# Performance work log

Hardware: AMD Instinct MI355X
Metric: run time of the kernel (lower is better)

Reference implementation:

```python
import jax, jax.numpy as jnp
import numpy as np

WS = 7          # window size per spatial dim
NH = 12         # num heads
DIM = 384       # channels
HD = DIM // NH  # head dim = 32
SCALE = HD ** -0.5
N = WS * WS * WS  # 343 tokens per window
B_ = 128        # windows * batch
NW = 64         # mask windows


def _relative_position_index():
    # Faithful replica of the torch __init__ (including indexing='xy' and the
    # 3*Ws[1]-1 / 2*Ws[1]-1 stride multipliers).
    c = np.arange(WS)
    coords = np.stack(np.meshgrid(c, c, c, indexing='xy'))  # (3, WS, WS, WS)
    cf = coords.reshape(3, -1)                               # (3, N)
    rel = (cf[:, :, None] - cf[:, None, :]).transpose(1, 2, 0).astype(np.int64)
    rel = rel + (WS - 1)
    rel[..., 0] *= 3 * WS - 1
    rel[..., 1] *= 2 * WS - 1
    return rel.sum(-1).astype(np.int32)  # (N, N)


def setup_inputs() -> dict:
    key = jax.random.key(0)
    ks = jax.random.split(key, 8)
    return {
        'skip': jax.random.normal(ks[0], (B_, N, DIM), jnp.float32),
        'x_up': jax.random.normal(ks[1], (B_, N, DIM), jnp.float32),
        'pos_embed': jax.random.normal(ks[2], (B_, N, DIM), jnp.float32),
        'mask': jax.random.normal(ks[3], (NW, N, N), jnp.float32),
        'w_kv': jax.random.normal(ks[4], (2 * DIM, DIM), jnp.float32) * 0.02,
        'b_kv': jnp.zeros((2 * DIM,), jnp.float32),
        'w_proj': jax.random.normal(ks[5], (DIM, DIM), jnp.float32) * 0.02,
        'b_proj': jnp.zeros((DIM,), jnp.float32),
        'bias_table': jax.random.normal(ks[6], ((2 * WS - 1) ** 3, NH), jnp.float32) * 0.02,
        'rpi': jnp.asarray(_relative_position_index()),
    }


def reference(skip, x_up, pos_embed, mask, w_kv, b_kv, w_proj, b_proj, bias_table, rpi):
    B, Ntok, C = skip.shape
    # kv projection from skip: (B, N, 2, H, d)
    kv = (skip @ w_kv.T + b_kv).reshape(B, Ntok, 2, NH, HD)
    k = kv[:, :, 0].transpose(0, 2, 1, 3)  # (B, H, N, d)
    v = kv[:, :, 1].transpose(0, 2, 1, 3)  # (B, H, N, d)
    q = x_up.reshape(B, Ntok, NH, HD).transpose(0, 2, 1, 3) * SCALE  # (B, H, N, d)
    attn = jnp.einsum('bhnd,bhmd->bhnm', q, k)  # (B, H, N, N)
    # relative position bias gather: (N, N, H) -> (H, N, N)
    bias = bias_table[rpi.reshape(-1)].reshape(Ntok, Ntok, NH).transpose(2, 0, 1)
    attn = attn + bias[None]
    # shifted-window mask add
    nW = mask.shape[0]
    attn = attn.reshape(B // nW, nW, NH, Ntok, Ntok) + mask[None, :, None]
    attn = jax.nn.softmax(attn.reshape(B, NH, Ntok, Ntok), axis=-1)
    x = jnp.einsum('bhnm,bhmd->bnhd', attn, v).reshape(B, Ntok, C)
    x = x + pos_embed
    return x @ w_proj.T + b_proj
```

## Files before the change

### kernel.cpp

```cpp
#include <hip/hip_runtime.h>

#define NTOK 343
#define NPAD 352
#define DIM 384
#define NHEAD 12
#define HDIM 32
#define NWIN 64
#define BATCH 128
#define SCALE 0.17677669529663687f
#define LOG2E 1.4426950408889634f
#define SCLG2 (0.17677669529663687f * 1.4426950408889634f)
#define NN 117649
#define MG 88
#define GSTRIDE 1372

typedef __attribute__((ext_vector_type(8))) short bf16x8;
typedef __attribute__((ext_vector_type(4))) short bf16x4;
typedef __attribute__((ext_vector_type(4))) float f32x4;
typedef __attribute__((ext_vector_type(4))) int i32x4;

static __device__ inline short f2bf(float f) {
  union { float f; unsigned u; } v; v.f = f;
  unsigned r = v.u + 0x7fffu + ((v.u >> 16) & 1u);
  return (short)(r >> 16);
}
static __device__ inline float bf2f(short s) {
  union { unsigned u; float f; } v; v.u = ((unsigned)(unsigned short)s) << 16;
  return v.f;
}
static __device__ inline int pack2rn(float lo, float hi) {
  union { float f; unsigned u; } a, b;
  a.f = lo; b.f = hi;
  unsigned au = a.u + 0x8000u;
  unsigned bu = b.u + 0x8000u;
  return (int)__builtin_amdgcn_perm(bu, au, 0x07060302u);
}
static __device__ inline short f2bfrn(float f) {
  union { float f; unsigned u; } v; v.f = f;
  return (short)((v.u + 0x8000u) >> 16);
}
static __device__ inline float fexp2(float x) {
  return __builtin_amdgcn_exp2f(x);
}

#define MFMA16(a, b, c) __builtin_amdgcn_mfma_f32_16x16x32_bf16((a), (b), (c), 0, 0, 0)

__global__ __launch_bounds__(256) void bias_pk_kernel(
    const float* __restrict__ table, const int* __restrict__ rpi,
    short* __restrict__ bias_b4) {
  int idx = blockIdx.x * 256 + threadIdx.x;
  const int total = NHEAD * MG * NTOK * 4;
  if (idx >= total) return;
  int r = idx & 3;
  int t = idx >> 2;
  int q = t % NTOK;
  int u = t / NTOK;
  int g = u % MG;
  int h = u / MG;
  int m = g * 4 + r;
  bias_b4[idx] = (m < NTOK) ? f2bf(table[rpi[q * NTOK + m] * NHEAD + h] * LOG2E)
                            : f2bf(-1e30f);
}

__global__ __launch_bounds__(256) void mask_pk_kernel(
    const float* __restrict__ in, short* __restrict__ mask_b4) {
  int idx = blockIdx.x * 256 + threadIdx.x;
  const int total = NWIN * MG * NTOK * 4;
  if (idx >= total) return;
  int r = idx & 3;
  int t = idx >> 2;
  int q = t % NTOK;
  int u = t / NTOK;
  int g = u % MG;
  int w = u / MG;
  int m = g * 4 + r;
  mask_b4[idx] = (m < NTOK) ? f2bf(in[(size_t)w * NN + q * NTOK + m] * LOG2E) : 0;
}

__global__ __launch_bounds__(256) void cvt_skip_kernel(
    const float* __restrict__ in, short* __restrict__ out, int n8) {
  int i = blockIdx.x * 256 + threadIdx.x;
  if (i >= n8) return;
  f32x4 a = *(const f32x4*)(in + (size_t)i * 8);
  f32x4 b = *(const f32x4*)(in + (size_t)i * 8 + 4);
  bf16x8 o;
#pragma unroll
  for (int j = 0; j < 4; ++j) {
    o[j] = f2bf(a[j]);
    o[j + 4] = f2bf(b[j]);
  }
  *(bf16x8*)(out + (size_t)i * 8) = o;
}

__global__ __launch_bounds__(256) void kv_proj_kernel(
    const short* __restrict__ Xbf, const float* __restrict__ W,
    const float* __restrict__ bkv, short* __restrict__ Kws,
    short* __restrict__ Vws) {
  __shared__ short As[128][40];
  __shared__ short Bs[128][40];
  const int L = blockIdx.x;
  const int xcd = L & 7;
  const int j8 = L >> 3;
  const int wg = ((xcd < 2) ? xcd * 258 : 516 + (xcd - 2) * 257) + j8;
  const int n0 = (wg % 6) * 128;
  const int m0 = (wg / 6) * 128;
  const int tid = threadIdx.x;
  const int lane = tid & 63;
  const int wave = tid >> 6;
  const int wm = (wave >> 1) * 64;
  const int wn = (wave & 1) * 64;
  const int lr = lane & 15;
  const int lk = (lane >> 4) * 8;
  const int c4 = (tid & 7) * 4;
  const int rbase = tid >> 3;
  const int arow = tid >> 2;
  const int acol8 = (tid & 3) * 8;
  const f32x4 zero4 = {0.f, 0.f, 0.f, 0.f};

  f32x4 acc[4][4];
#pragma unroll
  for (int m = 0; m < 4; ++m)
#pragma unroll
    for (int n = 0; n < 4; ++n) acc[m][n] = zero4;

  for (int kk = 0; kk < 12; ++kk) {
    __syncthreads();
    *(bf16x8*)(&As[arow][acol8]) =
        *(const bf16x8*)(Xbf + (size_t)(m0 + arow) * DIM + kk * 32 + acol8);
    *(bf16x8*)(&As[arow + 64][acol8]) =
        *(const bf16x8*)(Xbf + (size_t)(m0 + arow + 64) * DIM + kk * 32 + acol8);
#pragma unroll
    for (int i = 0; i < 4; ++i) {
      int row = rbase + i * 32;
      f32x4 v = *(const f32x4*)(W + (size_t)(n0 + row) * DIM + kk * 32 + c4);
      bf16x4 s4;
#pragma unroll
      for (int j = 0; j < 4; ++j) s4[j] = f2bf(v[j]);
      *(bf16x4*)(&Bs[row][c4]) = s4;
    }
    __syncthreads();
    bf16x8 af[4], bf[4];
#pragma unroll
    for (int m = 0; m < 4; ++m) af[m] = *(const bf16x8*)(&As[wm + m * 16 + lr][lk]);
#pragma unroll
    for (int n = 0; n < 4; ++n) bf[n] = *(const bf16x8*)(&Bs[wn + n * 16 + lr][lk]);
#pragma unroll
    for (int m = 0; m < 4; ++m)
#pragma unroll
      for (int n = 0; n < 4; ++n) acc[m][n] = MFMA16(af[m], bf[n], acc[m][n]);
  }

  const int rq = (lane >> 4) * 4;
#pragma unroll
  for (int n = 0; n < 4; ++n) {
    int gcol = n0 + wn + n * 16 + lr;
    float bias = bkv[gcol];
    int c = (gcol >= DIM) ? (gcol - DIM) : gcol;
    int h = c >> 5;
    int hd = c & 31;
    short* dst = (gcol < DIM) ? Kws : Vws;
#pragma unroll
    for (int m = 0; m < 4; ++m) {
#pragma unroll
      for (int r = 0; r < 4; ++r) {
        int grow = m0 + wm + m * 16 + rq + r;
        int bb = grow / NTOK;
        int tok = grow - bb * NTOK;
        dst[(((size_t)bb * NHEAD + h) * NTOK + tok) * HDIM + hd] =
            f2bf(acc[m][n][r] + bias);
      }
    }
  }
}

__global__ __launch_bounds__(256, 3) void attn_kernel(
    const float* __restrict__ x_up, const short* __restrict__ mask_b4,
    const short* __restrict__ bias_b4, const short* __restrict__ Kws,
    const short* __restrict__ Vws, const float* __restrict__ pos,
    short* __restrict__ attn_out) {
  __shared__ short Ksm[NPAD][40];
  __shared__ short Vp[HDIM][NPAD + 8];
  const int bid = blockIdx.x;
  const int xcd = bid & 7;
  const int jj = bid >> 3;
  const int win = xcd * 8 + jj / 24;
  const int rep = jj - (jj / 24) * 24;
  const int h = rep % NHEAD;
  const int b = win + ((rep >= NHEAD) ? 64 : 0);
  const int tid = threadIdx.x;
  const int wave = tid >> 6;
  const int lane = tid & 63;
  const int lr = lane & 15;
  const int lg = lane >> 4;
  const int koff = lg * 8;
  const int koff_s = koff ^ (lane & 8);
  const f32x4 zero4 = {0.f, 0.f, 0.f, 0.f};

  const short* Kb = Kws + ((size_t)b * NHEAD + h) * NTOK * HDIM;
  const short* Vb = Vws + ((size_t)b * NHEAD + h) * NTOK * HDIM;
  {
    const int c8 = (tid & 3) * 8;
    const int rb = tid >> 2;
    const bf16x8 z8 = {0, 0, 0, 0, 0, 0, 0, 0};
#pragma unroll
    for (int r0 = 0; r0 < 384; r0 += 64) {
      int row = r0 + rb;
      if (row < NPAD) {
        bf16x8 kv = z8;
        if (row < NTOK) kv = *(const bf16x8*)(Kb + row * HDIM + c8);
        *(bf16x8*)(&Ksm[row][c8 ^ (row & 8)]) = kv;
      }
    }
#pragma unroll
    for (int r0 = 0; r0 < 384; r0 += 64) {
      int row = r0 + rb;
      if (row < NPAD) {
        bf16x8 vv = z8;
        if (row < NTOK) vv = *(const bf16x8*)(Vb + row * HDIM + c8);
        int p = (row & ~31) | ((row & 12) << 1) | ((row & 16) >> 2) | (row & 3);
#pragma unroll
        for (int i = 0; i < 8; ++i)
          Vp[c8 + i][p ^ ((c8 + i) & 8)] = vv[i];
      }
    }
  }
  __syncthreads();

  for (int qt = 0; qt < 6; ++qt) {
    const int q0 = qt * 64 + wave * 16;
    if (q0 >= NTOK) continue;
    const int qn = q0 + lr;
    const int qidx = (qn < NTOK) ? qn : (NTOK - 1);
    bf16x8 qf;
    {
      const float* qp = x_up + ((size_t)b * NTOK + qidx) * DIM + h * HDIM + koff;
      f32x4 v0 = *(const f32x4*)qp;
      f32x4 v1 = *(const f32x4*)(qp + 4);
#pragma unroll
      for (int i = 0; i < 4; ++i) {
        qf[i] = f2bfrn(v0[i] * SCLG2);
        qf[i + 4] = f2bfrn(v1[i] * SCLG2);
      }
    }
    const short* bq = bias_b4 + (size_t)h * MG * GSTRIDE + (size_t)lg * GSTRIDE +
                      qidx * 4;
    const short* mq = mask_b4 + (size_t)win * MG * GSTRIDE + (size_t)lg * GSTRIDE +
                      qidx * 4;
    f32x4 s[22];
#pragma unroll
    for (int j = 0; j < 22; ++j) {
      bf16x4 bv = *(const bf16x4*)(bq + (size_t)j * 4 * GSTRIDE);
      bf16x4 mv = *(const bf16x4*)(mq + (size_t)j * 4 * GSTRIDE);
#pragma unroll
      for (int r = 0; r < 4; ++r) s[j][r] = bf2f(bv[r]) + bf2f(mv[r]);
    }
    __builtin_amdgcn_s_setprio(1);
#pragma unroll
    for (int j = 0; j < 22; ++j) {
      bf16x8 kf = *(const bf16x8*)(&Ksm[j * 16 + lr][koff_s]);
      s[j] = MFMA16(kf, qf, s[j]);
    }
    __builtin_amdgcn_s_setprio(0);
    f32x4 sum4 = zero4;
    i32x4 up4[11];
#pragma unroll
    for (int j = 0; j < 22; ++j) {
      f32x4 p;
#pragma unroll
      for (int r = 0; r < 4; ++r) p[r] = fexp2(s[j][r]);
      sum4 += p;
      up4[j >> 1][(j & 1) * 2 + 0] = pack2rn(p[0], p[1]);
      up4[j >> 1][(j & 1) * 2 + 1] = pack2rn(p[2], p[3]);
    }
    float sum = (sum4[0] + sum4[1]) + (sum4[2] + sum4[3]);
    sum += __shfl_xor(sum, 16);
    sum += __shfl_xor(sum, 32);
    const float inv = 1.0f / sum;

    f32x4 o0 = zero4;
    f32x4 o1 = zero4;
    __builtin_amdgcn_s_setprio(1);
#pragma unroll
    for (int kt = 0; kt < 11; ++kt) {
      bf16x8 pf = __builtin_bit_cast(bf16x8, up4[kt]);
      bf16x8 a0 = *(const bf16x8*)(&Vp[lr][kt * 32 + koff_s]);
      bf16x8 a1 = *(const bf16x8*)(&Vp[16 + lr][kt * 32 + koff_s]);
      o0 = MFMA16(a0, pf, o0);
      o1 = MFMA16(a1, pf, o1);
    }
    __builtin_amdgcn_s_setprio(0);
    if (qn < NTOK) {
      const float* pp = pos + ((size_t)b * NTOK + qn) * DIM + h * HDIM + 4 * lg;
      f32x4 p0 = *(const f32x4*)pp;
      f32x4 p1 = *(const f32x4*)(pp + 16);
      short* op = attn_out + ((size_t)b * NTOK + qn) * DIM + h * HDIM + 4 * lg;
      *(int*)(op + 0) = pack2rn(o0[0] * inv + p0[0], o0[1] * inv + p0[1]);
      *(int*)(op + 2) = pack2rn(o0[2] * inv + p0[2], o0[3] * inv + p0[3]);
      *(int*)(op + 16) = pack2rn(o1[0] * inv + p1[0], o1[1] * inv + p1[1]);
      *(int*)(op + 18) = pack2rn(o1[2] * inv + p1[2], o1[3] * inv + p1[3]);
    }
  }
}

__global__ __launch_bounds__(256) void out_proj_kernel(
    const short* __restrict__ Xa, const float* __restrict__ W,
    const float* __restrict__ bpr, float* __restrict__ out) {
  __shared__ short As[128][40];
  __shared__ short Bs[128][40];
  const int L = blockIdx.x;
  const int xcd = L & 7;
  const int j8 = L >> 3;
  const int wg = ((xcd < 5) ? xcd * 129 : 645 + (xcd - 5) * 128) + j8;
  const int n0 = (wg % 3) * 128;
  const int m0 = (wg / 3) * 128;
  const int tid = threadIdx.x;
  const int lane = tid & 63;
  const int wave = tid >> 6;
  const int wm = (wave >> 1) * 64;
  const int wn = (wave & 1) * 64;
  const int lr = lane & 15;
  const int lk = (lane >> 4) * 8;
  const int c4 = (tid & 7) * 4;
  const int rbase = tid >> 3;
  const int arow = tid >> 2;
  const int acol8 = (tid & 3) * 8;
  const f32x4 zero4 = {0.f, 0.f, 0.f, 0.f};

  f32x4 acc[4][4];
#pragma unroll
  for (int m = 0; m < 4; ++m)
#pragma unroll
    for (int n = 0; n < 4; ++n) acc[m][n] = zero4;

  for (int kk = 0; kk < 12; ++kk) {
    __syncthreads();
    *(bf16x8*)(&As[arow][acol8]) =
        *(const bf16x8*)(Xa + (size_t)(m0 + arow) * DIM + kk * 32 + acol8);
    *(bf16x8*)(&As[arow + 64][acol8]) =
        *(const bf16x8*)(Xa + (size_t)(m0 + arow + 64) * DIM + kk * 32 + acol8);
#pragma unroll
    for (int i = 0; i < 4; ++i) {
      int row = rbase + i * 32;
      f32x4 v = *(const f32x4*)(W + (size_t)(n0 + row) * DIM + kk * 32 + c4);
      bf16x4 s4;
#pragma unroll
      for (int j = 0; j < 4; ++j) s4[j] = f2bf(v[j]);
      *(bf16x4*)(&Bs[row][c4]) = s4;
    }
    __syncthreads();
    bf16x8 af[4], bf[4];
#pragma unroll
    for (int m = 0; m < 4; ++m) af[m] = *(const bf16x8*)(&As[wm + m * 16 + lr][lk]);
#pragma unroll
    for (int n = 0; n < 4; ++n) bf[n] = *(const bf16x8*)(&Bs[wn + n * 16 + lr][lk]);
#pragma unroll
    for (int m = 0; m < 4; ++m)
#pragma unroll
      for (int n = 0; n < 4; ++n) acc[m][n] = MFMA16(af[m], bf[n], acc[m][n]);
  }

  const int rq = (lane >> 4) * 4;
#pragma unroll
  for (int n = 0; n < 4; ++n) {
    int gcol = n0 + wn + n * 16 + lr;
    float bias = bpr[gcol];
#pragma unroll
    for (int m = 0; m < 4; ++m) {
#pragma unroll
      for (int r = 0; r < 4; ++r) {
        int grow = m0 + wm + m * 16 + rq + r;
        out[(size_t)grow * DIM + gcol] = acc[m][n][r] + bias;
      }
    }
  }
}

extern "C" void kernel_launch(void* const* d_in, const int* in_sizes, int n_in,
                              void* d_out, int out_size, void* d_ws, size_t ws_size,
                              hipStream_t stream) {
  const float* skip = (const float*)d_in[0];
  const float* x_up = (const float*)d_in[1];
  const float* pos = (const float*)d_in[2];
  const float* mask = (const float*)d_in[3];
  const float* w_kv = (const float*)d_in[4];
  const float* b_kv = (const float*)d_in[5];
  const float* w_proj = (const float*)d_in[6];
  const float* b_proj = (const float*)d_in[7];
  const float* bias_table = (const float*)d_in[8];
  const int* rpi = (const int*)d_in[9];
  float* out = (float*)d_out;

  char* ws = (char*)d_ws;
  const size_t kv_bytes = (size_t)BATCH * NHEAD * NTOK * HDIM * 2;
  const size_t bias_bytes = (size_t)NHEAD * MG * NTOK * 4 * 2;
  const size_t mask_bytes = (size_t)NWIN * MG * NTOK * 4 * 2;
  short* Kws = (short*)ws;
  short* Vws = (short*)(ws + kv_bytes);
  short* bias_b4 = (short*)(ws + 2 * kv_bytes);
  short* mask_b4 = (short*)(ws + 2 * kv_bytes + bias_bytes);
  short* skip_bf = (short*)(ws + 2 * kv_bytes + bias_bytes + mask_bytes);
  short* attn_ws = skip_bf;

  const int bias_total = NHEAD * MG * NTOK * 4;
  const int mask_total = NWIN * MG * NTOK * 4;
  const int n8 = BATCH * NTOK * DIM / 8;
  bias_pk_kernel<<<dim3((bias_total + 255) / 256), dim3(256), 0, stream>>>(
      bias_table, rpi, bias_b4);
  mask_pk_kernel<<<dim3((mask_total + 255) / 256), dim3(256), 0, stream>>>(
      mask, mask_b4);
  cvt_skip_kernel<<<dim3((n8 + 255) / 256), dim3(256), 0, stream>>>(
      skip, skip_bf, n8);
  kv_proj_kernel<<<dim3(2058), dim3(256), 0, stream>>>(skip_bf, w_kv, b_kv,
                                                       Kws, Vws);
  attn_kernel<<<dim3(BATCH * NHEAD), dim3(256), 0, stream>>>(
      x_up, mask_b4, bias_b4, Kws, Vws, pos, attn_ws);
  out_proj_kernel<<<dim3(1029), dim3(256), 0, stream>>>(attn_ws, w_proj,
                                                        b_proj, out);
}
```

Measured before the change: 280.3 us.

## Merge prep kernels, pre-convert weights to bf16, prefetch bias/mask tiles in attention

Replaces the three preprocessing launches with one combined prep kernel that also converts w_kv and w_proj to bf16 once. The projection GEMMs then load bf16 weight tiles directly instead of converting fp32 weights on every tile load. In the attention kernel, bias and mask values for the next query tile are loaded into registers while the current tile is still being computed, so global load latency is hidden. The cost is higher register pressure from the 44 prefetch registers, which may reduce occupancy, plus a little extra workspace.

```diff
diff --git a/kernel.cpp b/kernel.cpp
--- a/kernel.cpp
+++ b/kernel.cpp
@@ -14,19 +14,25 @@
 #define MG 88
 #define GSTRIDE 1372
 
+#define GB 5660
+#define GM 30184
+#define GS 8232
+#define GWK 144
+#define GWP 72
+
 typedef __attribute__((ext_vector_type(8))) short bf16x8;
 typedef __attribute__((ext_vector_type(4))) short bf16x4;
 typedef __attribute__((ext_vector_type(4))) float f32x4;
 typedef __attribute__((ext_vector_type(4))) int i32x4;
+typedef __attribute__((ext_vector_type(2))) int i32x2;
 
 static __device__ inline short f2bf(float f) {
   union { float f; unsigned u; } v; v.f = f;
   unsigned r = v.u + 0x7fffu + ((v.u >> 16) & 1u);
   return (short)(r >> 16);
 }
-static __device__ inline float bf2f(short s) {
-  union { unsigned u; float f; } v; v.u = ((unsigned)(unsigned short)s) << 16;
-  return v.f;
+static __device__ inline float asfu(unsigned u) {
+  union { unsigned u; float f; } v; v.u = u; return v.f;
 }
 static __device__ inline int pack2rn(float lo, float hi) {
   union { float f; unsigned u; } a, b;
@@ -45,41 +51,8 @@
 
 #define MFMA16(a, b, c) __builtin_amdgcn_mfma_f32_16x16x32_bf16((a), (b), (c), 0, 0, 0)
 
-__global__ __launch_bounds__(256) void bias_pk_kernel(
-    const float* __restrict__ table, const int* __restrict__ rpi,
-    short* __restrict__ bias_b4) {
-  int idx = blockIdx.x * 256 + threadIdx.x;
-  const int total = NHEAD * MG * NTOK * 4;
-  if (idx >= total) return;
-  int r = idx & 3;
-  int t = idx >> 2;
-  int q = t % NTOK;
-  int u = t / NTOK;
-  int g = u % MG;
-  int h = u / MG;
-  int m = g * 4 + r;
-  bias_b4[idx] = (m < NTOK) ? f2bf(table[rpi[q * NTOK + m] * NHEAD + h] * LOG2E)
-                            : f2bf(-1e30f);
-}
-
-__global__ __launch_bounds__(256) void mask_pk_kernel(
-    const float* __restrict__ in, short* __restrict__ mask_b4) {
-  int idx = blockIdx.x * 256 + threadIdx.x;
-  const int total = NWIN * MG * NTOK * 4;
-  if (idx >= total) return;
-  int r = idx & 3;
-  int t = idx >> 2;
-  int q = t % NTOK;
-  int u = t / NTOK;
-  int g = u % MG;
-  int w = u / MG;
-  int m = g * 4 + r;
-  mask_b4[idx] = (m < NTOK) ? f2bf(in[(size_t)w * NN + q * NTOK + m] * LOG2E) : 0;
-}
-
-__global__ __launch_bounds__(256) void cvt_skip_kernel(
-    const float* __restrict__ in, short* __restrict__ out, int n8) {
-  int i = blockIdx.x * 256 + threadIdx.x;
+static __device__ inline void cvt8(const float* __restrict__ in,
+                                   short* __restrict__ out, int i, int n8) {
   if (i >= n8) return;
   f32x4 a = *(const f32x4*)(in + (size_t)i * 8);
   f32x4 b = *(const f32x4*)(in + (size_t)i * 8 + 4);
@@ -92,8 +65,48 @@
   *(bf16x8*)(out + (size_t)i * 8) = o;
 }
 
+__global__ __launch_bounds__(256) void prep_kernel(
+    const float* __restrict__ table, const int* __restrict__ rpi,
+    short* __restrict__ bias_b4, const float* __restrict__ mask,
+    short* __restrict__ mask_b4, const float* __restrict__ skip,
+    short* __restrict__ skip_bf, const float* __restrict__ wkv,
+    short* __restrict__ wkv_bf, const float* __restrict__ wproj,
+    short* __restrict__ wproj_bf) {
+  const int g = blockIdx.x;
+  const int tid = threadIdx.x;
+  if (g < GB) {
+    int idx = g * 256 + tid;
+    if (idx >= NHEAD * MG * NTOK * 4) return;
+    int r = idx & 3;
+    int t = idx >> 2;
+    int q = t % NTOK;
+    int u = t / NTOK;
+    int gg = u % MG;
+    int h = u / MG;
+    int m = gg * 4 + r;
+    bias_b4[idx] = (m < NTOK) ? f2bf(table[rpi[q * NTOK + m] * NHEAD + h] * LOG2E)
+                              : f2bf(-1e30f);
+  } else if (g < GB + GM) {
+    int idx = (g - GB) * 256 + tid;
+    int r = idx & 3;
+    int t = idx >> 2;
+    int q = t % NTOK;
+    int u = t / NTOK;
+    int gg = u % MG;
+    int w = u / MG;
+    int m = gg * 4 + r;
+    mask_b4[idx] = (m < NTOK) ? f2bf(mask[(size_t)w * NN + q * NTOK + m] * LOG2E) : 0;
+  } else if (g < GB + GM + GS) {
+    cvt8(skip, skip_bf, (g - GB - GM) * 256 + tid, BATCH * NTOK * DIM / 8);
+  } else if (g < GB + GM + GS + GWK) {
+    cvt8(wkv, wkv_bf, (g - GB - GM - GS) * 256 + tid, 2 * DIM * DIM / 8);
+  } else {
+    cvt8(wproj, wproj_bf, (g - GB - GM - GS - GWK) * 256 + tid, DIM * DIM / 8);
+  }
+}
+
 __global__ __launch_bounds__(256) void kv_proj_kernel(
-    const short* __restrict__ Xbf, const float* __restrict__ W,
+    const short* __restrict__ Xbf, const short* __restrict__ Wbf,
     const float* __restrict__ bkv, short* __restrict__ Kws,
     short* __restrict__ Vws) {
   __shared__ short As[128][40];
@@ -111,8 +124,6 @@
   const int wn = (wave & 1) * 64;
   const int lr = lane & 15;
   const int lk = (lane >> 4) * 8;
-  const int c4 = (tid & 7) * 4;
-  const int rbase = tid >> 3;
   const int arow = tid >> 2;
   const int acol8 = (tid & 3) * 8;
   const f32x4 zero4 = {0.f, 0.f, 0.f, 0.f};
@@ -129,15 +140,10 @@
         *(const bf16x8*)(Xbf + (size_t)(m0 + arow) * DIM + kk * 32 + acol8);
     *(bf16x8*)(&As[arow + 64][acol8]) =
         *(const bf16x8*)(Xbf + (size_t)(m0 + arow + 64) * DIM + kk * 32 + acol8);
-#pragma unroll
-    for (int i = 0; i < 4; ++i) {
-      int row = rbase + i * 32;
-      f32x4 v = *(const f32x4*)(W + (size_t)(n0 + row) * DIM + kk * 32 + c4);
-      bf16x4 s4;
-#pragma unroll
-      for (int j = 0; j < 4; ++j) s4[j] = f2bf(v[j]);
-      *(bf16x4*)(&Bs[row][c4]) = s4;
-    }
+    *(bf16x8*)(&Bs[arow][acol8]) =
+        *(const bf16x8*)(Wbf + (size_t)(n0 + arow) * DIM + kk * 32 + acol8);
+    *(bf16x8*)(&Bs[arow + 64][acol8]) =
+        *(const bf16x8*)(Wbf + (size_t)(n0 + arow + 64) * DIM + kk * 32 + acol8);
     __syncthreads();
     bf16x8 af[4], bf[4];
 #pragma unroll
@@ -226,6 +232,20 @@
   }
   __syncthreads();
 
+  const size_t bbase = (size_t)h * MG * GSTRIDE + (size_t)lg * GSTRIDE;
+  const size_t mbase = (size_t)win * MG * GSTRIDE + (size_t)lg * GSTRIDE;
+  i32x2 Rb[22], Rm[22];
+  {
+    int qi = wave * 16 + lr;
+    const short* bq = bias_b4 + bbase + (size_t)qi * 4;
+    const short* mq = mask_b4 + mbase + (size_t)qi * 4;
+#pragma unroll
+    for (int j = 0; j < 22; ++j) {
+      Rb[j] = *(const i32x2*)(bq + (size_t)j * 4 * GSTRIDE);
+      Rm[j] = *(const i32x2*)(mq + (size_t)j * 4 * GSTRIDE);
+    }
+  }
+
   for (int qt = 0; qt < 6; ++qt) {
     const int q0 = qt * 64 + wave * 16;
     if (q0 >= NTOK) continue;
@@ -242,17 +262,15 @@
         qf[i + 4] = f2bfrn(v1[i] * SCLG2);
       }
     }
-    const short* bq = bias_b4 + (size_t)h * MG * GSTRIDE + (size_t)lg * GSTRIDE +
-                      qidx * 4;
-    const short* mq = mask_b4 + (size_t)win * MG * GSTRIDE + (size_t)lg * GSTRIDE +
-                      qidx * 4;
     f32x4 s[22];
 #pragma unroll
     for (int j = 0; j < 22; ++j) {
-      bf16x4 bv = *(const bf16x4*)(bq + (size_t)j * 4 * GSTRIDE);
-      bf16x4 mv = *(const bf16x4*)(mq + (size_t)j * 4 * GSTRIDE);
-#pragma unroll
-      for (int r = 0; r < 4; ++r) s[j][r] = bf2f(bv[r]) + bf2f(mv[r]);
+      unsigned b0 = (unsigned)Rb[j][0], b1 = (unsigned)Rb[j][1];
+      unsigned c0 = (unsigned)Rm[j][0], c1 = (unsigned)Rm[j][1];
+      s[j][0] = asfu(b0 << 16) + asfu(c0 << 16);
+      s[j][1] = asfu(b0 & 0xFFFF0000u) + asfu(c0 & 0xFFFF0000u);
+      s[j][2] = asfu(b1 << 16) + asfu(c1 << 16);
+      s[j][3] = asfu(b1 & 0xFFFF0000u) + asfu(c1 & 0xFFFF0000u);
     }
     __builtin_amdgcn_s_setprio(1);
 #pragma unroll
@@ -271,6 +289,20 @@
       sum4 += p;
       up4[j >> 1][(j & 1) * 2 + 0] = pack2rn(p[0], p[1]);
       up4[j >> 1][(j & 1) * 2 + 1] = pack2rn(p[2], p[3]);
+    }
+    if (qt < 5) {
+      const int q0n = q0 + 64;
+      if (q0n < NTOK) {
+        int qin = q0n + lr;
+        if (qin >= NTOK) qin = NTOK - 1;
+        const short* bq = bias_b4 + bbase + (size_t)qin * 4;
+        const short* mq = mask_b4 + mbase + (size_t)qin * 4;
+#pragma unroll
+        for (int j = 0; j < 22; ++j) {
+          Rb[j] = *(const i32x2*)(bq + (size_t)j * 4 * GSTRIDE);
+          Rm[j] = *(const i32x2*)(mq + (size_t)j * 4 * GSTRIDE);
+        }
+      }
     }
     float sum = (sum4[0] + sum4[1]) + (sum4[2] + sum4[3]);
     sum += __shfl_xor(sum, 16);
@@ -303,7 +335,7 @@
 }
 
 __global__ __launch_bounds__(256) void out_proj_kernel(
-    const short* __restrict__ Xa, const float* __restrict__ W,
+    const short* __restrict__ Xa, const short* __restrict__ Wbf,
     const float* __restrict__ bpr, float* __restrict__ out) {
   __shared__ short As[128][40];
   __shared__ short Bs[128][40];
@@ -320,8 +352,6 @@
   const int wn = (wave & 1) * 64;
   const int lr = lane & 15;
   const int lk = (lane >> 4) * 8;
-  const int c4 = (tid & 7) * 4;
-  const int rbase = tid >> 3;
   const int arow = tid >> 2;
   const int acol8 = (tid & 3) * 8;
   const f32x4 zero4 = {0.f, 0.f, 0.f, 0.f};
@@ -338,15 +368,10 @@
         *(const bf16x8*)(Xa + (size_t)(m0 + arow) * DIM + kk * 32 + acol8);
     *(bf16x8*)(&As[arow + 64][acol8]) =
         *(const bf16x8*)(Xa + (size_t)(m0 + arow + 64) * DIM + kk * 32 + acol8);
-#pragma unroll
-    for (int i = 0; i < 4; ++i) {
-      int row = rbase + i * 32;
-      f32x4 v = *(const f32x4*)(W + (size_t)(n0 + row) * DIM + kk * 32 + c4);
-      bf16x4 s4;
-#pragma unroll
-      for (int j = 0; j < 4; ++j) s4[j] = f2bf(v[j]);
-      *(bf16x4*)(&Bs[row][c4]) = s4;
-    }
+    *(bf16x8*)(&Bs[arow][acol8]) =
+        *(const bf16x8*)(Wbf + (size_t)(n0 + arow) * DIM + kk * 32 + acol8);
+    *(bf16x8*)(&Bs[arow + 64][acol8]) =
+        *(const bf16x8*)(Wbf + (size_t)(n0 + arow + 64) * DIM + kk * 32 + acol8);
     __syncthreads();
     bf16x8 af[4], bf[4];
 #pragma unroll
@@ -394,26 +419,25 @@
   const size_t kv_bytes = (size_t)BATCH * NHEAD * NTOK * HDIM * 2;
   const size_t bias_bytes = (size_t)NHEAD * MG * NTOK * 4 * 2;
   const size_t mask_bytes = (size_t)NWIN * MG * NTOK * 4 * 2;
+  const size_t wkv_bytes = (size_t)2 * DIM * DIM * 2;
+  const size_t wpr_bytes = (size_t)DIM * DIM * 2;
   short* Kws = (short*)ws;
   short* Vws = (short*)(ws + kv_bytes);
   short* bias_b4 = (short*)(ws + 2 * kv_bytes);
   short* mask_b4 = (short*)(ws + 2 * kv_bytes + bias_bytes);
-  short* skip_bf = (short*)(ws + 2 * kv_bytes + bias_bytes + mask_bytes);
+  short* wkv_bf = (short*)(ws + 2 * kv_bytes + bias_bytes + mask_bytes);
+  short* wproj_bf = (short*)(ws + 2 * kv_bytes + bias_bytes + mask_bytes + wkv_bytes);
+  short* skip_bf = (short*)(ws + 2 * kv_bytes + bias_bytes + mask_bytes +
+                            wkv_bytes + wpr_bytes);
   short* attn_ws = skip_bf;
 
-  const int bias_total = NHEAD * MG * NTOK * 4;
-  const int mask_total = NWIN * MG * NTOK * 4;
-  const int n8 = BATCH * NTOK * DIM / 8;
-  bias_pk_kernel<<<dim3((bias_total + 255) / 256), dim3(256), 0, stream>>>(
-      bias_table, rpi, bias_b4);
-  mask_pk_kernel<<<dim3((mask_total + 255) / 256), dim3(256), 0, stream>>>(
-      mask, mask_b4);
-  cvt_skip_kernel<<<dim3((n8 + 255) / 256), dim3(256), 0, stream>>>(
-      skip, skip_bf, n8);
-  kv_proj_kernel<<<dim3(2058), dim3(256), 0, stream>>>(skip_bf, w_kv, b_kv,
+  prep_kernel<<<dim3(GB + GM + GS + GWK + GWP), dim3(256), 0, stream>>>(
+      bias_table, rpi, bias_b4, mask, mask_b4, skip, skip_bf, w_kv, wkv_bf,
+      w_proj, wproj_bf);
+  kv_proj_kernel<<<dim3(2058), dim3(256), 0, stream>>>(skip_bf, wkv_bf, b_kv,
                                                        Kws, Vws);
   attn_kernel<<<dim3(BATCH * NHEAD), dim3(256), 0, stream>>>(
       x_up, mask_b4, bias_b4, Kws, Vws, pos, attn_ws);
-  out_proj_kernel<<<dim3(1029), dim3(256), 0, stream>>>(attn_ws, w_proj,
+  out_proj_kernel<<<dim3(1029), dim3(256), 0, stream>>>(attn_ws, wproj_bf,
                                                         b_proj, out);
 }
```

Result: slower. 528.7 us (+88.6%).
